# Kernel optimization log

Hardware: AMD Instinct MI355X
Metric: run time of the kernel (lower is better)

Reference implementation:

```python
import jax, jax.numpy as jnp
import numpy as np

H, HKV, D, BS, NSEL, WIN = 32, 8, 64, 64, 16, 512
N_REP = H // HKV


def precompute_freqs(dim, max_seq_len, theta=10000.0):
    inv = 1.0 / theta ** (np.arange(0, dim, 2, dtype=np.float32) / dim)
    t = np.arange(max_seq_len, dtype=np.float32)
    return jnp.asarray(np.outer(t, inv))  # (S, dim//2)


def apply_rope(x, freqs):
    # x: (B, T, H, D)
    T = x.shape[1]
    xr = x.reshape(x.shape[:-1] + (-1, 2))
    cos = jnp.cos(freqs[:T])[None, :, None, :]
    sin = jnp.sin(freqs[:T])[None, :, None, :]
    x0, x1 = xr[..., 0], xr[..., 1]
    out = jnp.stack([x0 * cos - x1 * sin, x0 * sin + x1 * cos], axis=-1)
    return out.reshape(x.shape)


def setup_inputs() -> dict:
    key = jax.random.key(0)
    ks = jax.random.split(key, 9)
    d_model = 2048
    s = lambda fan_in: 1.0 / np.sqrt(fan_in)
    return {
        "x": jax.random.normal(ks[0], (1, 2048, d_model), jnp.float32),
        "W_q": jax.random.normal(ks[1], (d_model, H * D), jnp.float32) * s(d_model),
        "W_k": jax.random.normal(ks[2], (d_model, HKV * D), jnp.float32) * s(d_model),
        "W_v": jax.random.normal(ks[3], (d_model, HKV * D), jnp.float32) * s(d_model),
        "W_o": jax.random.normal(ks[4], (H * D, d_model), jnp.float32) * s(H * D),
        "W_ck": jax.random.normal(ks[5], (BS * D, D), jnp.float32) * s(BS * D),
        "W_cv": jax.random.normal(ks[6], (BS * D, D), jnp.float32) * s(BS * D),
        "W_imp": jax.random.normal(ks[7], (D, 1), jnp.float32) * s(D),
        "W_gate": jax.random.normal(ks[8], (d_model, 3), jnp.float32) * s(d_model),
    }


def reference(x, W_q, W_k, W_v, W_o, W_ck, W_cv, W_imp, W_gate):
    B, T, _ = x.shape
    S = T  # no kv_cache
    scale = 1.0 / np.sqrt(D)
    freqs = precompute_freqs(D, T)

    q = apply_rope((x @ W_q).reshape(B, T, H, D), freqs)
    k = apply_rope((x @ W_k).reshape(B, T, HKV, D), freqs)
    v = (x @ W_v).reshape(B, T, HKV, D)
    q = q.transpose(0, 2, 1, 3)  # (B,H,T,D)
    k = k.transpose(0, 2, 1, 3)  # (B,HKV,S,D)
    v = v.transpose(0, 2, 1, 3)

    # --- compressed-block branch ---
    nb = S // BS
    kb = k[:, :, : nb * BS].reshape(B, HKV, nb, BS * D)
    vb = v[:, :, : nb * BS].reshape(B, HKV, nb, BS * D)
    kc = jnp.repeat(kb @ W_ck, N_REP, axis=1)  # (B,H,nb,D)
    vc = jnp.repeat(vb @ W_cv, N_REP, axis=1)
    a_c = jax.nn.softmax(jnp.einsum('bhtd,bhnd->bhtn', q, kc) * scale, axis=-1)
    out_c = jnp.einsum('bhtn,bhnd->bhtd', a_c, vc)

    # GQA expansion shared by select / sliding branches
    kx = jnp.repeat(k, N_REP, axis=1)
    vx = jnp.repeat(v, N_REP, axis=1)

    # --- 'selected' branch (reference computes top-k indices but discards them;
    # attention is full dense unmasked softmax, faithfully reproduced) ---
    k_mean = k[:, :, : nb * BS].reshape(B, HKV, nb, BS, D).mean(axis=3)
    scores = (k_mean @ W_imp)[..., 0]
    _top = jax.lax.top_k(scores, NSEL)  # dead code in original; kept for faithfulness
    a_s = jax.nn.softmax(jnp.einsum('bhtd,bhsd->bhts', q, kx) * scale, axis=-1)
    out_s = jnp.einsum('bhts,bhsd->bhtd', a_s, vx)

    # --- sliding-window branch (dense scores + mask, as in original) ---
    logits = jnp.einsum('bhtd,bhsd->bhts', q, kx) * scale
    i = jnp.arange(T)[:, None]
    j = jnp.arange(S)[None, :]
    allowed = (j <= S - T + i) & (j >= S - T + i - WIN + 1)
    logits = jnp.where(allowed[None, None], logits, -jnp.inf)
    a_w = jnp.nan_to_num(jax.nn.softmax(logits, axis=-1))
    out_w = jnp.einsum('bhts,bhsd->bhtd', a_w, vx)

    # --- gated combine ---
    gates = jax.nn.softmax(x @ W_gate, axis=-1)  # (B,T,3)
    stacked = jnp.stack(
        [out_c.transpose(0, 2, 1, 3), out_s.transpose(0, 2, 1, 3), out_w.transpose(0, 2, 1, 3)],
        axis=3,
    )  # (B,T,H,3,D)
    out = (stacked * gates[:, :, None, :, None]).sum(axis=3).reshape(B, T, H * D)
    return out @ W_o
```

## Files before the change

kernel.cpp:

```cpp
#include <hip/hip_runtime.h>
#include <cmath>

typedef unsigned short u16;
typedef unsigned int u32;
typedef __attribute__((ext_vector_type(8))) __bf16 bf16x8;
typedef __attribute__((ext_vector_type(8))) u16 u16x8;
typedef __attribute__((ext_vector_type(4))) float f32x4;
typedef __attribute__((ext_vector_type(4))) u16 u16x4;

#define MFMA16(acc, a, b) (acc) = __builtin_amdgcn_mfma_f32_16x16x32_bf16((a), (b), (acc), 0, 0, 0)

__device__ __forceinline__ u16 f2bf(float x) {
  union { float f; u32 u; } c; c.f = x;
  u32 r = (c.u + 0x7FFFu + ((c.u >> 16) & 1u)) >> 16;
  return (u16)r;
}
__device__ __forceinline__ float bf2f(u16 b) {
  union { u32 u; float f; } c; c.u = ((u32)b) << 16;
  return c.f;
}
__device__ __forceinline__ float rowmax16(float v) {
#pragma unroll
  for (int m = 1; m < 16; m <<= 1) v = fmaxf(v, __shfl_xor(v, m));
  return v;
}
__device__ __forceinline__ float rowsum16(float v) {
#pragma unroll
  for (int m = 1; m < 16; m <<= 1) v += __shfl_xor(v, m);
  return v;
}
__device__ __forceinline__ void gload16(const u16* g, u16* l) {
  __builtin_amdgcn_global_load_lds(
      (const __attribute__((address_space(1))) void*)(g),
      (__attribute__((address_space(3))) void*)(l), 16, 0, 0);
}
__device__ __forceinline__ float exp2_asm(float x) {
  float r;
  asm("v_exp_f32 %0, %1\n\ts_nop 0" : "=v"(r) : "v"(x));
  return r;
}
__device__ __forceinline__ u32 cvtpk(float a, float b) {
  u32 r;
  asm("v_cvt_pk_bf16_f32 %0, %1, %2" : "=v"(r) : "v"(a), "v"(b));
  return r;
}
__device__ __forceinline__ u16x8 bc_u(bf16x8 v) { union { bf16x8 b; u16x8 u; } c; c.b = v; return c.u; }
__device__ __forceinline__ bf16x8 bc_b(u16x8 v) { union { u16x8 u; bf16x8 b; } c; c.u = v; return c.b; }

__global__ void freqs_kernel(float* __restrict__ ct, float* __restrict__ st) {
  int idx = blockIdx.x * 256 + threadIdx.x;
  int t = idx >> 5, i = idx & 31;
  float inv = 1.0f / powf(10000.0f, (float)i / 32.0f);
  float a = (float)t * inv;
  float sv, cv;
  sincosf(a, &sv, &cv);
  ct[idx] = cv;
  st[idx] = sv;
}

__global__ void cvt_x_kernel(const float* __restrict__ in, u16* __restrict__ out) {
  int idx = (blockIdx.x * 256 + threadIdx.x) * 4;
  f32x4 v = *(const f32x4*)(in + idx);
  u16x4 o;
  o[0] = f2bf(v[0]); o[1] = f2bf(v[1]); o[2] = f2bf(v[2]); o[3] = f2bf(v[3]);
  *(u16x4*)(out + idx) = o;
}

__global__ __launch_bounds__(256) void trcvt_kernel(const float* __restrict__ W,
                                                    u16* __restrict__ Wt, int K, int N) {
  __shared__ u16 t_lds[64][65];
  int ntx = N >> 6;
  int kt = (blockIdx.x / ntx) * 64, nt = (blockIdx.x % ntx) * 64;
  int tx = threadIdx.x & 63, ty4 = threadIdx.x >> 6;
#pragma unroll 4
  for (int yy = 0; yy < 16; ++yy) {
    int k = kt + ty4 * 16 + yy;
    t_lds[ty4 * 16 + yy][tx] = f2bf(W[(size_t)k * N + nt + tx]);
  }
  __syncthreads();
#pragma unroll 4
  for (int yy = 0; yy < 16; ++yy) {
    int n = nt + ty4 * 16 + yy;
    Wt[(size_t)n * K + kt + tx] = t_lds[tx][ty4 * 16 + yy];
  }
}

__global__ __launch_bounds__(256) void gemm_bt_kernel(const u16* __restrict__ A,
                                                      const u16* __restrict__ Bt,
                                                      float* __restrict__ C,
                                                      int M, int N, int K) {
  __shared__ __align__(16) u16 As[128 * 64];
  __shared__ __align__(16) u16 Bs[128 * 64];
  const int tid = threadIdx.x;
  const int lane = tid & 63;
  const int w = tid >> 6;
  const int lr = lane & 15;
  const int lg = lane >> 4;
  const int lk8 = lg * 8;
  const int gx = gridDim.x;
  const int nwg = gx * gridDim.y;
  const int flat = blockIdx.y * gx + blockIdx.x;
  const int qq = nwg >> 3;
  const int swz = (flat & 7) * qq + (flat >> 3);
  const int brow = (swz % gx) * 128;
  const int bcol = (swz / gx) * 128;
  const int wr = (w >> 1) * 64;
  const int wc = (w & 1) * 64;

  const f32x4 zero4 = {0.f, 0.f, 0.f, 0.f};
  f32x4 acc[4][4];
#pragma unroll
  for (int m = 0; m < 4; ++m)
#pragma unroll
    for (int n = 0; n < 4; ++n) acc[m][n] = zero4;

  const int srow = tid >> 3;
  const int scol = (tid & 7) * 8;
  const u16* Ab = A + (size_t)(brow + srow) * K + scol;
  const u16* Bb = Bt + (size_t)(bcol + srow) * K + scol;

  for (int k0 = 0; k0 < K; k0 += 64) {
    __syncthreads();
#pragma unroll
    for (int it = 0; it < 4; ++it) {
      gload16(Ab + (size_t)it * 32 * K + k0, &As[tid * 8 + it * 2048]);
      gload16(Bb + (size_t)it * 32 * K + k0, &Bs[tid * 8 + it * 2048]);
    }
    __syncthreads();
#pragma unroll
    for (int kk = 0; kk < 2; ++kk) {
      bf16x8 af[4], bv[4];
#pragma unroll
      for (int m = 0; m < 4; ++m)
        af[m] = *(const bf16x8*)&As[(wr + m * 16 + lr) * 64 + kk * 32 + lk8];
#pragma unroll
      for (int n = 0; n < 4; ++n)
        bv[n] = *(const bf16x8*)&Bs[(wc + n * 16 + lr) * 64 + kk * 32 + lk8];
#pragma unroll
      for (int m = 0; m < 4; ++m)
#pragma unroll
        for (int n = 0; n < 4; ++n) MFMA16(acc[m][n], af[m], bv[n]);
    }
  }
#pragma unroll
  for (int m = 0; m < 4; ++m) {
#pragma unroll
    for (int rr = 0; rr < 4; ++rr) {
      int row = brow + wr + m * 16 + lg * 4 + rr;
#pragma unroll
      for (int n = 0; n < 4; ++n)
        C[(size_t)row * N + bcol + wc + n * 16 + lr] = acc[m][n][rr];
    }
  }
}

__global__ void rope_q_kernel(const float* __restrict__ qkv, const float* __restrict__ ct,
                              const float* __restrict__ st, u16* __restrict__ qb) {
  int idx = blockIdx.x * 256 + threadIdx.x;
  int i = idx & 31, hh = (idx >> 5) & 31, t = idx >> 10;
  float x0 = qkv[(size_t)t * 3072 + hh * 64 + 2 * i];
  float x1 = qkv[(size_t)t * 3072 + hh * 64 + 2 * i + 1];
  float c = ct[t * 32 + i], s = st[t * 32 + i];
  size_t o = ((size_t)hh * 2048 + t) * 64 + 2 * i;
  qb[o] = f2bf((x0 * c - x1 * s) * 0.125f);
  qb[o + 1] = f2bf((x0 * s + x1 * c) * 0.125f);
}
__global__ void rope_k_kernel(const float* __restrict__ qkv, const float* __restrict__ ct,
                              const float* __restrict__ st, u16* __restrict__ kb) {
  int idx = blockIdx.x * 256 + threadIdx.x;
  int i = idx & 31, hh = (idx >> 5) & 7, t = idx >> 8;
  float x0 = qkv[(size_t)t * 3072 + 2048 + hh * 64 + 2 * i];
  float x1 = qkv[(size_t)t * 3072 + 2048 + hh * 64 + 2 * i + 1];
  float c = ct[t * 32 + i], s = st[t * 32 + i];
  size_t o = ((size_t)hh * 2048 + t) * 64 + 2 * i;
  kb[o] = f2bf(x0 * c - x1 * s);
  kb[o + 1] = f2bf(x0 * s + x1 * c);
}
__global__ __launch_bounds__(256) void vtrans_kernel(const float* __restrict__ qkv,
                                                     u16* __restrict__ vbr,
                                                     u16* __restrict__ vb2) {
  __shared__ u16 tl[64][72];
  int hk = blockIdx.y, t0 = blockIdx.x * 64;
  int tx = threadIdx.x & 63, ty = threadIdx.x >> 6;
#pragma unroll 4
  for (int yy = 0; yy < 16; ++yy) {
    int row = ty * 16 + yy;
    u16 b = f2bf(qkv[(size_t)(t0 + row) * 3072 + 2560 + hk * 64 + tx]);
    tl[row][tx] = b;
    vbr[((size_t)hk * 2048 + t0 + row) * 64 + tx] = b;
  }
  __syncthreads();
  u16* dst = vb2 + (size_t)hk * 64 * 2048 + t0;
#pragma unroll 4
  for (int yy = 0; yy < 16; ++yy)
    dst[(size_t)(ty * 16 + yy) * 2048 + tx] = tl[tx][ty * 16 + yy];
}

__global__ __launch_bounds__(256) void gates_kernel(const float* __restrict__ x,
                                                    const float* __restrict__ Wg,
                                                    float* __restrict__ g) {
  int t = blockIdx.x * 4 + (threadIdx.x >> 6);
  int lane = threadIdx.x & 63;
  const float* xr = x + (size_t)t * 2048;
  float a0 = 0, a1 = 0, a2 = 0;
  for (int d = lane; d < 2048; d += 64) {
    float xv = xr[d];
    a0 = fmaf(xv, Wg[d * 3 + 0], a0);
    a1 = fmaf(xv, Wg[d * 3 + 1], a1);
    a2 = fmaf(xv, Wg[d * 3 + 2], a2);
  }
#pragma unroll
  for (int msk = 1; msk < 64; msk <<= 1) {
    a0 += __shfl_xor(a0, msk);
    a1 += __shfl_xor(a1, msk);
    a2 += __shfl_xor(a2, msk);
  }
  if (lane == 0) {
    float m = fmaxf(a0, fmaxf(a1, a2));
    float e0 = __expf(a0 - m), e1 = __expf(a1 - m), e2 = __expf(a2 - m);
    float inv = 1.f / (e0 + e1 + e2);
    g[t * 3 + 0] = e0 * inv; g[t * 3 + 1] = e1 * inv; g[t * 3 + 2] = e2 * inv;
  }
}

__global__ __launch_bounds__(256) void cgemm_kernel(const u16* __restrict__ kB,
                                                    const u16* __restrict__ vbr,
                                                    const float* __restrict__ Wck,
                                                    const float* __restrict__ Wcv,
                                                    float* __restrict__ kc,
                                                    float* __restrict__ vc) {
  __shared__ float red[4][64];
  int b = blockIdx.x;
  bool isv = b >= 256;
  int blk = b & 255;
  const u16* src = (isv ? vbr : kB) + (size_t)blk * 4096;
  const float* W = isv ? Wcv : Wck;
  float* out = (isv ? vc : kc) + (size_t)blk * 64;
  int lane = threadIdx.x & 63, w = threadIdx.x >> 6;
  int base = w * 1024;
  float acc0 = 0.f, acc1 = 0.f;
  for (int i = 0; i < 1024; i += 8) {
    u16x8 s8 = *(const u16x8*)(src + base + i);
#pragma unroll
    for (int j = 0; j < 8; j += 2) {
      acc0 = fmaf(bf2f(s8[j]), W[(size_t)(base + i + j) * 64 + lane], acc0);
      acc1 = fmaf(bf2f(s8[j + 1]), W[(size_t)(base + i + j + 1) * 64 + lane], acc1);
    }
  }
  red[w][lane] = acc0 + acc1;
  __syncthreads();
  if (w == 0)
    out[lane] = red[0][lane] + red[1][lane] + red[2][lane] + red[3][lane];
}

__global__ __launch_bounds__(256) void attn_kernel(
    const u16* __restrict__ qb, const u16* __restrict__ kb, const u16* __restrict__ vb2,
    const float* __restrict__ kcf, const float* __restrict__ vcf,
    const float* __restrict__ gf, u16* __restrict__ comb) {
  __shared__ __align__(16) u16 k_lds[64 * 64];
  __shared__ __align__(16) u16 vt_lds[64 * 64];
  __shared__ __align__(16) u16 kc_lds[32 * 72];
  __shared__ __align__(16) u16 vtc_lds[64 * 40];
  __shared__ __align__(16) u16 p_lds[4][16 * 72];

  const int tid = threadIdx.x;
  const int lane = tid & 63;
  const int w = tid >> 6;
  const int lr = lane & 15;
  const int lg = lane >> 4;
  const int lk8 = lg * 8;
  const int h = blockIdx.y;
  const int hk = h >> 2;
  const int t0 = blockIdx.x * 64;
  const int tw = t0 + w * 16;
  const f32x4 zero4 = {0.f, 0.f, 0.f, 0.f};
  const float LOG2E = 1.44269504f;
  const float LN2 = 0.69314718f;
  const float THR = 11.5416f;

  bf16x8 qf0, qf1;
  {
    const u16* qrow = qb + ((size_t)h * 2048 + (tw + lr)) * 64;
    qf0 = *(const bf16x8*)(qrow + lk8);
    qf1 = *(const bf16x8*)(qrow + 32 + lk8);
  }

  for (int e = tid; e < 32 * 64; e += 256) {
    int n = e >> 6, d = e & 63;
    kc_lds[n * 72 + d] = f2bf(kcf[((size_t)hk * 32 + n) * 64 + d]);
    vtc_lds[d * 40 + n] = f2bf(vcf[((size_t)hk * 32 + n) * 64 + d]);
  }

  const int lin1 = 256 + tid;
  const int row0 = tid >> 3, sl0 = (tid & 7) ^ (row0 & 7);
  const int row1 = lin1 >> 3, sl1 = (lin1 & 7) ^ (row1 & 7);
  const u16* kS0 = kb + ((size_t)hk * 2048 + row0) * 64 + sl0 * 8;
  const u16* kS1 = kb + ((size_t)hk * 2048 + row1) * 64 + sl1 * 8;
  const u16* vS0 = vb2 + ((size_t)hk * 64 + row0) * 2048 + sl0 * 8;
  const u16* vS1 = vb2 + ((size_t)hk * 64 + row1) * 2048 + sl1 * 8;
  u16* kD0 = &k_lds[tid * 8];
  u16* kD1 = &k_lds[lin1 * 8];
  u16* vD0 = &vt_lds[tid * 8];
  u16* vD1 = &vt_lds[lin1 * 8];

  const int sA = ((0 + lg) ^ (lr & 7)) * 8;
  const int sB = ((4 + lg) ^ (lr & 7)) * 8;

  f32x4 acc_s[4], acc_w[4];
#pragma unroll
  for (int n = 0; n < 4; ++n) { acc_s[n] = zero4; acc_w[n] = zero4; }
  float m2[4], lsr[4], lwr[4];
#pragma unroll
  for (int r = 0; r < 4; ++r) { m2[r] = -1e30f; lsr[r] = 0.f; lwr[r] = 0.f; }

#pragma unroll 1
  for (int c = 0; c < 32; ++c) {
    const int s0 = c * 64;
    __syncthreads();
    gload16(kS0 + (size_t)s0 * 64, kD0);
    gload16(kS1 + (size_t)s0 * 64, kD1);
    gload16(vS0 + s0, vD0);
    gload16(vS1 + s0, vD1);
    __syncthreads();

    f32x4 sc[4];
#pragma unroll
    for (int cb = 0; cb < 4; ++cb) {
      f32x4 z = zero4;
      const int rb = (cb * 16 + lr) * 64;
      bf16x8 b0 = *(const bf16x8*)&k_lds[rb + sA];
      bf16x8 b1 = *(const bf16x8*)&k_lds[rb + sB];
      MFMA16(z, qf0, b0);
      MFMA16(z, qf1, b1);
      sc[cb] = z;
    }

    const bool winAct = (s0 <= tw + 15) && (s0 + 63 >= tw - 511);
    const int dbase = tw + lg * 4 - s0 - lr;

#pragma unroll
    for (int r = 0; r < 4; ++r) {
      float mxl = fmaxf(fmaxf(sc[0][r], sc[1][r]), fmaxf(sc[2][r], sc[3][r]));
      float thr_raw = (m2[r] + THR) * LN2;
      if (__any(mxl > thr_raw)) {
        float mnew = fmaxf(m2[r], rowmax16(mxl) * LOG2E);
        float corr = exp2_asm(m2[r] - mnew);
        m2[r] = mnew;
        lsr[r] *= corr;
        lwr[r] *= corr;
#pragma unroll
        for (int n = 0; n < 4; ++n) { acc_s[n][r] *= corr; acc_w[n][r] *= corr; }
      }
      float pv0 = exp2_asm(fmaf(sc[0][r], LOG2E, -m2[r]));
      float pv1 = exp2_asm(fmaf(sc[1][r], LOG2E, -m2[r]));
      float pv2 = exp2_asm(fmaf(sc[2][r], LOG2E, -m2[r]));
      float pv3 = exp2_asm(fmaf(sc[3][r], LOG2E, -m2[r]));
      lsr[r] += (pv0 + pv1) + (pv2 + pv3);
      if (winAct) {
        int d0 = dbase + r;
        float s = 0.f;
        s += ((u32)d0 < 512u) ? pv0 : 0.f;
        s += ((u32)(d0 - 16) < 512u) ? pv1 : 0.f;
        s += ((u32)(d0 - 32) < 512u) ? pv2 : 0.f;
        s += ((u32)(d0 - 48) < 512u) ? pv3 : 0.f;
        lwr[r] += s;
      }
      u32 pk01 = cvtpk(pv0, pv1), pk23 = cvtpk(pv2, pv3);
      u16* pr = &p_lds[w][(lg * 4 + r) * 72 + lr];
      pr[0] = (u16)pk01;
      pr[16] = (u16)(pk01 >> 16);
      pr[32] = (u16)pk23;
      pr[48] = (u16)(pk23 >> 16);
    }
    asm volatile("s_waitcnt lgkmcnt(0)" ::: "memory");
    bf16x8 ap0 = *(const bf16x8*)&p_lds[w][lr * 72 + lk8];
    bf16x8 ap1 = *(const bf16x8*)&p_lds[w][lr * 72 + 32 + lk8];

    bf16x8 aw0 = ap0, aw1 = ap1;
    if (winAct) {
      const int base0 = (tw + lr) - (s0 + lk8);
      u16x8 a0 = bc_u(ap0), a1 = bc_u(ap1);
      u16x8 z0, z1;
#pragma unroll
      for (int j = 0; j < 8; ++j) {
        z0[j] = ((u32)(base0 - j) < 512u) ? a0[j] : (u16)0;
        z1[j] = ((u32)(base0 - 32 - j) < 512u) ? a1[j] : (u16)0;
      }
      aw0 = bc_b(z0);
      aw1 = bc_b(z1);
    }

#pragma unroll
    for (int n = 0; n < 4; ++n) {
      const int rb = (n * 16 + lr) * 64;
      bf16x8 bv0 = *(const bf16x8*)&vt_lds[rb + sA];
      bf16x8 bv1 = *(const bf16x8*)&vt_lds[rb + sB];
      MFMA16(acc_s[n], ap0, bv0);
      MFMA16(acc_s[n], ap1, bv1);
      if (winAct) {
        MFMA16(acc_w[n], aw0, bv0);
        MFMA16(acc_w[n], aw1, bv1);
      }
    }
  }

  f32x4 accc[4];
  float lcv[4];
  {
    f32x4 sc0 = zero4, sc1 = zero4;
#pragma unroll
    for (int kk = 0; kk < 2; ++kk) {
      bf16x8 b0 = *(const bf16x8*)&kc_lds[(0 * 16 + lr) * 72 + kk * 32 + lk8];
      bf16x8 b1 = *(const bf16x8*)&kc_lds[(1 * 16 + lr) * 72 + kk * 32 + lk8];
      bf16x8 qk = kk ? qf1 : qf0;
      MFMA16(sc0, qk, b0);
      MFMA16(sc1, qk, b1);
    }
#pragma unroll
    for (int r = 0; r < 4; ++r) {
      float a = sc0[r], b = sc1[r];
      float m = rowmax16(fmaxf(a, b));
      float p0 = __expf(a - m), p1 = __expf(b - m);
      lcv[r] = rowsum16(p0 + p1);
      p_lds[w][(lg * 4 + r) * 72 + lr] = f2bf(p0);
      p_lds[w][(lg * 4 + r) * 72 + 16 + lr] = f2bf(p1);
    }
    asm volatile("s_waitcnt lgkmcnt(0)" ::: "memory");
    bf16x8 ap = *(const bf16x8*)&p_lds[w][lr * 72 + lk8];
#pragma unroll
    for (int n = 0; n < 4; ++n) {
      f32x4 z = zero4;
      bf16x8 bv = *(const bf16x8*)&vtc_lds[(n * 16 + lr) * 40 + lk8];
      MFMA16(z, ap, bv);
      accc[n] = z;
    }
  }

#pragma unroll
  for (int r = 0; r < 4; ++r) {
    float ls = rowsum16(lsr[r]);
    float lw = rowsum16(lwr[r]);
    int t = tw + lg * 4 + r;
    float g0 = gf[t * 3 + 0], g1 = gf[t * 3 + 1], g2 = gf[t * 3 + 2];
    float wc_ = g0 / lcv[r];
    float ws_ = g1 / ls;
    float ww_ = g2 / lw;
#pragma unroll
    for (int n = 0; n < 4; ++n) {
      float val = accc[n][r] * wc_ + acc_s[n][r] * ws_ + acc_w[n][r] * ww_;
      comb[(size_t)t * 2048 + h * 64 + n * 16 + lr] = f2bf(val);
    }
  }
}

extern "C" void kernel_launch(void* const* d_in, const int* in_sizes, int n_in,
                              void* d_out, int out_size, void* d_ws, size_t ws_size,
                              hipStream_t stream) {
  (void)in_sizes; (void)n_in; (void)out_size;
  const float* x   = (const float*)d_in[0];
  const float* Wq  = (const float*)d_in[1];
  const float* Wk  = (const float*)d_in[2];
  const float* Wv  = (const float*)d_in[3];
  const float* Wo  = (const float*)d_in[4];
  const float* Wck = (const float*)d_in[5];
  const float* Wcv = (const float*)d_in[6];
  const float* Wg  = (const float*)d_in[8];
  float* out = (float*)d_out;
  char* ws = (char*)d_ws;

  constexpr size_t OXB   = 0;
  constexpr size_t OWT   = OXB  + 8388608;
  constexpr size_t OWOT  = OWT  + 12582912;
  constexpr size_t OQKV  = OWOT + 8388608;
  constexpr size_t OQB   = OQKV + 25165824;
  constexpr size_t OKB   = OQB  + 8388608;
  constexpr size_t OVB   = OKB  + 2097152;
  constexpr size_t OCT   = OVB  + 2097152;
  constexpr size_t OST   = OCT  + 262144;
  constexpr size_t OKC   = OST  + 262144;
  constexpr size_t OVC   = OKC  + 65536;
  constexpr size_t OG    = OVC  + 65536;
  constexpr size_t OCOMB = OG   + 24576;
  constexpr size_t TOTAL = OCOMB + 8388608;
  if (ws_size < TOTAL) return;

  u16* xb    = (u16*)(ws + OXB);
  u16* WT    = (u16*)(ws + OWT);
  u16* WoT   = (u16*)(ws + OWOT);
  float* qkv = (float*)(ws + OQKV);
  u16* qB    = (u16*)(ws + OQB);
  u16* kB    = (u16*)(ws + OKB);
  u16* vB2   = (u16*)(ws + OVB);
  float* ct  = (float*)(ws + OCT);
  float* st  = (float*)(ws + OST);
  float* kc  = (float*)(ws + OKC);
  float* vc  = (float*)(ws + OVC);
  float* gg  = (float*)(ws + OG);
  u16* comb  = (u16*)(ws + OCOMB);
  u16* vbr   = comb;

  freqs_kernel<<<dim3(256), dim3(256), 0, stream>>>(ct, st);
  cvt_x_kernel<<<dim3(4096), dim3(256), 0, stream>>>(x, xb);
  trcvt_kernel<<<dim3(1024), dim3(256), 0, stream>>>(Wq, WT, 2048, 2048);
  trcvt_kernel<<<dim3(256),  dim3(256), 0, stream>>>(Wk, WT + (size_t)2048 * 2048, 2048, 512);
  trcvt_kernel<<<dim3(256),  dim3(256), 0, stream>>>(Wv, WT + (size_t)2560 * 2048, 2048, 512);
  trcvt_kernel<<<dim3(1024), dim3(256), 0, stream>>>(Wo, WoT, 2048, 2048);

  gemm_bt_kernel<<<dim3(16, 24), dim3(256), 0, stream>>>(xb, WT, qkv, 2048, 3072, 2048);

  rope_q_kernel<<<dim3(8192), dim3(256), 0, stream>>>(qkv, ct, st, qB);
  rope_k_kernel<<<dim3(2048), dim3(256), 0, stream>>>(qkv, ct, st, kB);
  vtrans_kernel<<<dim3(32, 8), dim3(256), 0, stream>>>(qkv, vbr, vB2);
  gates_kernel<<<dim3(512), dim3(256), 0, stream>>>(x, Wg, gg);

  cgemm_kernel<<<dim3(512), dim3(256), 0, stream>>>(kB, vbr, Wck, Wcv, kc, vc);

  attn_kernel<<<dim3(32, 32), dim3(256), 0, stream>>>(qB, kB, vB2, kc, vc, gg, comb);

  gemm_bt_kernel<<<dim3(16, 16), dim3(256), 0, stream>>>(comb, WoT, out, 2048, 2048, 2048);
}
```

Baseline: 293.5 us.

## Double-buffer K/V tiles in attention loop and read compressed KV from global

The attention kernel now double-buffers the K and V^T LDS tiles, prefetching chunk c+1 while chunk c is computed, and keeps one barrier per iteration instead of two. The compressed-branch K/V tiles are no longer staged in LDS; they are read straight from global memory and converted in registers. This frees LDS for the second buffer. The P scratch tile switches from padded rows to an XOR swizzle, and the online-softmax rescale check is merged into one wave-wide vote across all four rows. s_setprio hints are placed around the MFMA sections to favour matrix issue, at the cost of more LDS for two buffers and scattered global loads in the epilogue.

```diff
diff --git a/kernel.cpp b/kernel.cpp
--- a/kernel.cpp
+++ b/kernel.cpp
@@ -46,6 +46,14 @@
 }
 __device__ __forceinline__ u16x8 bc_u(bf16x8 v) { union { bf16x8 b; u16x8 u; } c; c.b = v; return c.u; }
 __device__ __forceinline__ bf16x8 bc_b(u16x8 v) { union { u16x8 u; bf16x8 b; } c; c.u = v; return c.b; }
+__device__ __forceinline__ bf16x8 pack8(f32x4 a, f32x4 b) {
+  union { u32 w[4]; bf16x8 v; } c;
+  c.w[0] = cvtpk(a[0], a[1]);
+  c.w[1] = cvtpk(a[2], a[3]);
+  c.w[2] = cvtpk(b[0], b[1]);
+  c.w[3] = cvtpk(b[2], b[3]);
+  return c.v;
+}
 
 __global__ void freqs_kernel(float* __restrict__ ct, float* __restrict__ st) {
   int idx = blockIdx.x * 256 + threadIdx.x;
@@ -257,11 +265,9 @@
     const u16* __restrict__ qb, const u16* __restrict__ kb, const u16* __restrict__ vb2,
     const float* __restrict__ kcf, const float* __restrict__ vcf,
     const float* __restrict__ gf, u16* __restrict__ comb) {
-  __shared__ __align__(16) u16 k_lds[64 * 64];
-  __shared__ __align__(16) u16 vt_lds[64 * 64];
-  __shared__ __align__(16) u16 kc_lds[32 * 72];
-  __shared__ __align__(16) u16 vtc_lds[64 * 40];
-  __shared__ __align__(16) u16 p_lds[4][16 * 72];
+  __shared__ __align__(16) u16 k_lds[2][64 * 64];
+  __shared__ __align__(16) u16 vt_lds[2][64 * 64];
+  __shared__ __align__(16) u16 p_lds[4][16 * 64];
 
   const int tid = threadIdx.x;
   const int lane = tid & 63;
@@ -275,7 +281,6 @@
   const int tw = t0 + w * 16;
   const f32x4 zero4 = {0.f, 0.f, 0.f, 0.f};
   const float LOG2E = 1.44269504f;
-  const float LN2 = 0.69314718f;
   const float THR = 11.5416f;
 
   bf16x8 qf0, qf1;
@@ -283,12 +288,6 @@
     const u16* qrow = qb + ((size_t)h * 2048 + (tw + lr)) * 64;
     qf0 = *(const bf16x8*)(qrow + lk8);
     qf1 = *(const bf16x8*)(qrow + 32 + lk8);
-  }
-
-  for (int e = tid; e < 32 * 64; e += 256) {
-    int n = e >> 6, d = e & 63;
-    kc_lds[n * 72 + d] = f2bf(kcf[((size_t)hk * 32 + n) * 64 + d]);
-    vtc_lds[d * 40 + n] = f2bf(vcf[((size_t)hk * 32 + n) * 64 + d]);
   }
 
   const int lin1 = 256 + tid;
@@ -298,10 +297,6 @@
   const u16* kS1 = kb + ((size_t)hk * 2048 + row1) * 64 + sl1 * 8;
   const u16* vS0 = vb2 + ((size_t)hk * 64 + row0) * 2048 + sl0 * 8;
   const u16* vS1 = vb2 + ((size_t)hk * 64 + row1) * 2048 + sl1 * 8;
-  u16* kD0 = &k_lds[tid * 8];
-  u16* kD1 = &k_lds[lin1 * 8];
-  u16* vD0 = &vt_lds[tid * 8];
-  u16* vD1 = &vt_lds[lin1 * 8];
 
   const int sA = ((0 + lg) ^ (lr & 7)) * 8;
   const int sB = ((4 + lg) ^ (lr & 7)) * 8;
@@ -312,38 +307,53 @@
   float m2[4], lsr[4], lwr[4];
 #pragma unroll
   for (int r = 0; r < 4; ++r) { m2[r] = -1e30f; lsr[r] = 0.f; lwr[r] = 0.f; }
+
+#define STAGE(cc)                                                      \
+  {                                                                    \
+    const int b_ = (cc) & 1;                                           \
+    gload16(kS0 + (size_t)(cc) * 4096, &k_lds[b_][tid * 8]);           \
+    gload16(kS1 + (size_t)(cc) * 4096, &k_lds[b_][2048 + tid * 8]);    \
+    gload16(vS0 + (cc) * 64, &vt_lds[b_][tid * 8]);                    \
+    gload16(vS1 + (cc) * 64, &vt_lds[b_][2048 + tid * 8]);             \
+  }
+
+  STAGE(0);
+  __syncthreads();
 
 #pragma unroll 1
   for (int c = 0; c < 32; ++c) {
     const int s0 = c * 64;
-    __syncthreads();
-    gload16(kS0 + (size_t)s0 * 64, kD0);
-    gload16(kS1 + (size_t)s0 * 64, kD1);
-    gload16(vS0 + s0, vD0);
-    gload16(vS1 + s0, vD1);
-    __syncthreads();
+    const u16* kbuf = k_lds[c & 1];
+    const u16* vbuf = vt_lds[c & 1];
+    if (c < 31) STAGE(c + 1);
 
     f32x4 sc[4];
+    __builtin_amdgcn_s_setprio(1);
 #pragma unroll
     for (int cb = 0; cb < 4; ++cb) {
       f32x4 z = zero4;
       const int rb = (cb * 16 + lr) * 64;
-      bf16x8 b0 = *(const bf16x8*)&k_lds[rb + sA];
-      bf16x8 b1 = *(const bf16x8*)&k_lds[rb + sB];
+      bf16x8 b0 = *(const bf16x8*)&kbuf[rb + sA];
+      bf16x8 b1 = *(const bf16x8*)&kbuf[rb + sB];
       MFMA16(z, qf0, b0);
       MFMA16(z, qf1, b1);
       sc[cb] = z;
     }
+    __builtin_amdgcn_s_setprio(0);
 
     const bool winAct = (s0 <= tw + 15) && (s0 + 63 >= tw - 511);
     const int dbase = tw + lg * 4 - s0 - lr;
 
-#pragma unroll
-    for (int r = 0; r < 4; ++r) {
-      float mxl = fmaxf(fmaxf(sc[0][r], sc[1][r]), fmaxf(sc[2][r], sc[3][r]));
-      float thr_raw = (m2[r] + THR) * LN2;
-      if (__any(mxl > thr_raw)) {
-        float mnew = fmaxf(m2[r], rowmax16(mxl) * LOG2E);
+    float mxl[4];
+#pragma unroll
+    for (int r = 0; r < 4; ++r)
+      mxl[r] = fmaxf(fmaxf(sc[0][r], sc[1][r]), fmaxf(sc[2][r], sc[3][r]));
+    float dmax = fmaxf(fmaxf(fmaf(mxl[0], LOG2E, -m2[0]), fmaf(mxl[1], LOG2E, -m2[1])),
+                       fmaxf(fmaf(mxl[2], LOG2E, -m2[2]), fmaf(mxl[3], LOG2E, -m2[3])));
+    if (__any(dmax > THR)) {
+#pragma unroll
+      for (int r = 0; r < 4; ++r) {
+        float mnew = fmaxf(m2[r], rowmax16(mxl[r]) * LOG2E);
         float corr = exp2_asm(m2[r] - mnew);
         m2[r] = mnew;
         lsr[r] *= corr;
@@ -351,6 +361,10 @@
 #pragma unroll
         for (int n = 0; n < 4; ++n) { acc_s[n][r] *= corr; acc_w[n][r] *= corr; }
       }
+    }
+
+#pragma unroll
+    for (int r = 0; r < 4; ++r) {
       float pv0 = exp2_asm(fmaf(sc[0][r], LOG2E, -m2[r]));
       float pv1 = exp2_asm(fmaf(sc[1][r], LOG2E, -m2[r]));
       float pv2 = exp2_asm(fmaf(sc[2][r], LOG2E, -m2[r]));
@@ -366,15 +380,19 @@
         lwr[r] += s;
       }
       u32 pk01 = cvtpk(pv0, pv1), pk23 = cvtpk(pv2, pv3);
-      u16* pr = &p_lds[w][(lg * 4 + r) * 72 + lr];
-      pr[0] = (u16)pk01;
-      pr[16] = (u16)(pk01 >> 16);
-      pr[32] = (u16)pk23;
-      pr[48] = (u16)(pk23 >> 16);
+      const int prow = lg * 4 + r;
+      const int pb = prow * 64 + (lr & 7);
+      const int rh = prow & 7;
+      const int shi = lr >> 3;
+      u16* pl = p_lds[w];
+      pl[pb + ((0 + shi) ^ rh) * 8] = (u16)pk01;
+      pl[pb + ((2 + shi) ^ rh) * 8] = (u16)(pk01 >> 16);
+      pl[pb + ((4 + shi) ^ rh) * 8] = (u16)pk23;
+      pl[pb + ((6 + shi) ^ rh) * 8] = (u16)(pk23 >> 16);
     }
     asm volatile("s_waitcnt lgkmcnt(0)" ::: "memory");
-    bf16x8 ap0 = *(const bf16x8*)&p_lds[w][lr * 72 + lk8];
-    bf16x8 ap1 = *(const bf16x8*)&p_lds[w][lr * 72 + 32 + lk8];
+    bf16x8 ap0 = *(const bf16x8*)&p_lds[w][lr * 64 + sA];
+    bf16x8 ap1 = *(const bf16x8*)&p_lds[w][lr * 64 + sB];
 
     bf16x8 aw0 = ap0, aw1 = ap1;
     if (winAct) {
@@ -390,11 +408,12 @@
       aw1 = bc_b(z1);
     }
 
+    __builtin_amdgcn_s_setprio(1);
 #pragma unroll
     for (int n = 0; n < 4; ++n) {
       const int rb = (n * 16 + lr) * 64;
-      bf16x8 bv0 = *(const bf16x8*)&vt_lds[rb + sA];
-      bf16x8 bv1 = *(const bf16x8*)&vt_lds[rb + sB];
+      bf16x8 bv0 = *(const bf16x8*)&vbuf[rb + sA];
+      bf16x8 bv1 = *(const bf16x8*)&vbuf[rb + sB];
       MFMA16(acc_s[n], ap0, bv0);
       MFMA16(acc_s[n], ap1, bv1);
       if (winAct) {
@@ -402,7 +421,11 @@
         MFMA16(acc_w[n], aw1, bv1);
       }
     }
-  }
+    __builtin_amdgcn_s_setprio(0);
+
+    __syncthreads();
+  }
+#undef STAGE
 
   f32x4 accc[4];
   float lcv[4];
@@ -410,8 +433,10 @@
     f32x4 sc0 = zero4, sc1 = zero4;
 #pragma unroll
     for (int kk = 0; kk < 2; ++kk) {
-      bf16x8 b0 = *(const bf16x8*)&kc_lds[(0 * 16 + lr) * 72 + kk * 32 + lk8];
-      bf16x8 b1 = *(const bf16x8*)&kc_lds[(1 * 16 + lr) * 72 + kk * 32 + lk8];
+      const float* kr0 = kcf + ((size_t)hk * 32 + 0 * 16 + lr) * 64 + kk * 32 + lk8;
+      const float* kr1 = kcf + ((size_t)hk * 32 + 1 * 16 + lr) * 64 + kk * 32 + lk8;
+      bf16x8 b0 = pack8(*(const f32x4*)kr0, *(const f32x4*)(kr0 + 4));
+      bf16x8 b1 = pack8(*(const f32x4*)kr1, *(const f32x4*)(kr1 + 4));
       bf16x8 qk = kk ? qf1 : qf0;
       MFMA16(sc0, qk, b0);
       MFMA16(sc1, qk, b1);
@@ -422,17 +447,26 @@
       float m = rowmax16(fmaxf(a, b));
       float p0 = __expf(a - m), p1 = __expf(b - m);
       lcv[r] = rowsum16(p0 + p1);
-      p_lds[w][(lg * 4 + r) * 72 + lr] = f2bf(p0);
-      p_lds[w][(lg * 4 + r) * 72 + 16 + lr] = f2bf(p1);
+      u32 pk = cvtpk(p0, p1);
+      const int prow = lg * 4 + r;
+      const int pb = prow * 64 + (lr & 7);
+      const int rh = prow & 7;
+      const int shi = lr >> 3;
+      u16* pl = p_lds[w];
+      pl[pb + ((0 + shi) ^ rh) * 8] = (u16)pk;
+      pl[pb + ((2 + shi) ^ rh) * 8] = (u16)(pk >> 16);
     }
     asm volatile("s_waitcnt lgkmcnt(0)" ::: "memory");
-    bf16x8 ap = *(const bf16x8*)&p_lds[w][lr * 72 + lk8];
-#pragma unroll
-    for (int n = 0; n < 4; ++n) {
+    bf16x8 ap = *(const bf16x8*)&p_lds[w][lr * 64 + sA];
+#pragma unroll
+    for (int nb = 0; nb < 4; ++nb) {
+      u16x8 bb;
+#pragma unroll
+      for (int j = 0; j < 8; ++j)
+        bb[j] = f2bf(vcf[((size_t)hk * 32 + lk8 + j) * 64 + nb * 16 + lr]);
       f32x4 z = zero4;
-      bf16x8 bv = *(const bf16x8*)&vtc_lds[(n * 16 + lr) * 40 + lk8];
-      MFMA16(z, ap, bv);
-      accc[n] = z;
+      MFMA16(z, ap, bc_b(bb));
+      accc[nb] = z;
     }
   }
 
```

After: 282.2 us. -3.8%, faster.
